# Performance work log

Hardware: AMD Instinct MI355X
Metric: run time of the kernel (lower is better)

Reference implementation:

```python
import jax, jax.numpy as jnp
import numpy as np

N_U = 8192
N_C = 8192
D_IN = 32
D_HID = 32  # hidden_dim == output_dim (required by the concat->Linear shape)


def _glorot(key, fan_in, fan_out):
    r = np.sqrt(6.0 / (fan_in + fan_out)).astype(np.float32)
    return jax.random.uniform(key, (fan_in, fan_out), jnp.float32, -r, r)


def setup_inputs() -> dict:
    key = jax.random.key(0)
    ks = jax.random.split(key, 12)
    X_U = jax.random.normal(ks[0], (N_U, D_IN), jnp.float32)
    X_C = jax.random.normal(ks[1], (N_C, D_IN), jnp.float32)
    adj_uu = jax.random.uniform(ks[2], (N_U, N_U), jnp.float32)
    adj_uc = jax.random.uniform(ks[3], (N_U, N_C), jnp.float32)
    adj_cc = jax.random.uniform(ks[4], (N_C, N_C), jnp.float32)
    weight_s = _glorot(ks[5], D_IN, D_HID)          # GCN_S.weight (shared for uu and cc)
    proj_u = _glorot(ks[6], D_IN, D_HID)            # GCN_C.projection_u
    proj_c = _glorot(ks[7], D_IN, D_HID)            # GCN_C.projection_c (unused in fwd math)
    weight_c = _glorot(ks[8], D_HID, D_HID)         # GCN_C.weight
    W_lin = jax.random.normal(ks[9], (D_IN + D_HID, D_HID), jnp.float32) * 0.05  # Linear, no bias
    a_vec = jax.random.normal(ks[10], (D_HID, 1), jnp.float32) * 0.05            # attention vector
    return {"X_U": X_U, "X_C": X_C, "adj_uu": adj_uu, "adj_uc": adj_uc, "adj_cc": adj_cc,
            "weight_s": weight_s, "proj_u": proj_u, "proj_c": proj_c,
            "weight_c": weight_c, "W_lin": W_lin, "a_vec": a_vec}


def gcn_s(adj, x, w):
    # D^-1/2 A D^-1/2 (X W), with D = 1 + rowsum(A); expressed as broadcast scaling
    dinv = jax.lax.rsqrt(1.0 + jnp.sum(adj, axis=1))  # [N]
    support = x @ w                                    # [N, d]
    return dinv[:, None] * (adj @ (dinv[:, None] * support))


def gcn_c(adj, x_u, p_u, w):
    # Du^-1/2 A Dc^-1/2 ((X_U P_u) W); projected_c is computed but unused upstream
    du = jax.lax.rsqrt(jnp.sum(adj, axis=1))  # [N_u]
    dc = jax.lax.rsqrt(jnp.sum(adj, axis=0))  # [N_c]
    support = (x_u @ p_u) @ w                  # [N_u, d]
    return du[:, None] * (adj @ (dc[:, None] * support))  # wait: see note below


def gcn_c_correct(adj, x_u, p_u, w):
    # norm_adj = diag(du) @ adj @ diag(dc)  -> [N_u, N_c]; output = norm_adj @ support ([N_u,d])
    # Actually original multiplies [N_u,N_c] norm_adj by support built from X_U [N_u,d]:
    # this only typechecks when N_u == N_c (as in the repo's usage). We keep that math.
    du = jax.lax.rsqrt(jnp.sum(adj, axis=1))
    dc = jax.lax.rsqrt(jnp.sum(adj, axis=0))
    support = (x_u @ p_u) @ w
    return du[:, None] * (adj @ (dc[:, None] * support))


def reference(X_U, X_C, adj_uu, adj_uc, adj_cc, weight_s, proj_u, proj_c, weight_c, W_lin, a_vec):
    node_embed_u = gcn_s(adj_uu, X_U, weight_s)            # [N_u, d]
    node_embed_c1 = gcn_s(adj_cc, X_C, weight_s)           # [N_c, d]
    node_embed_c2 = gcn_c_correct(adj_uc, X_U, proj_u, weight_c)  # [N_c, d]

    a_tau_1 = jax.nn.relu(jnp.concatenate([node_embed_c1, X_C], axis=-1) @ W_lin) @ a_vec  # [N_c,1]
    a_tau_2 = jax.nn.relu(jnp.concatenate([node_embed_c2, X_C], axis=-1) @ W_lin) @ a_vec  # [N_c,1]
    e_tau = jax.nn.softmax(jnp.concatenate([a_tau_1, a_tau_2], axis=1), axis=1)            # [N_c,2]

    Y_c = e_tau[:, 0:1] * node_embed_c1
    Y_u = e_tau[:, 1:2] * node_embed_c2
    node_embed_c = Y_c + Y_u
    return (node_embed_u, node_embed_c, Y_c, Y_u)
```

## Files before the change

### kernel.cpp

```cpp
#include <hip/hip_runtime.h>
#include <hip/hip_bf16.h>

#define N_NODES 8192

typedef __attribute__((ext_vector_type(8))) short short8;
typedef __attribute__((ext_vector_type(4))) float floatx4;

__device__ inline unsigned short f2bf(float f) {
  unsigned int u = __float_as_uint(f);
  u = (u + 0x7FFFu + ((u >> 16) & 1u)) >> 16;
  return (unsigned short)u;
}

__device__ inline short8 cvt8(const float4 lo, const float4 hi) {
  short8 r;
  r[0] = (short)f2bf(lo.x); r[1] = (short)f2bf(lo.y);
  r[2] = (short)f2bf(lo.z); r[3] = (short)f2bf(lo.w);
  r[4] = (short)f2bf(hi.x); r[5] = (short)f2bf(hi.y);
  r[6] = (short)f2bf(hi.z); r[7] = (short)f2bf(hi.w);
  return r;
}

__device__ inline float waveSum(float s) {
#pragma unroll
  for (int off = 32; off >= 1; off >>= 1) s += __shfl_xor(s, off, 64);
  return s;
}

__device__ inline void acc4(float4& a, const float4 b) {
  a.x += b.x; a.y += b.y; a.z += b.z; a.w += b.w;
}
__device__ inline float hsum4(const float4 v) { return v.x + v.y + v.z + v.w; }

__global__ __launch_bounds__(256) void k_rowsum(const float* __restrict__ A,
                                                float* __restrict__ dv) {
  int w = threadIdx.x >> 6, l = threadIdx.x & 63;
  long row = (long)blockIdx.x * 4 + w;
  const float* rp = A + row * N_NODES + 4 * l;
  float s = 0.f;
#pragma unroll 2
  for (int i = 0; i < 32; i += 4) {
    float4 v0 = *(const float4*)(rp + 256 * (i + 0));
    float4 v1 = *(const float4*)(rp + 256 * (i + 1));
    float4 v2 = *(const float4*)(rp + 256 * (i + 2));
    float4 v3 = *(const float4*)(rp + 256 * (i + 3));
    s += hsum4(v0) + hsum4(v1) + hsum4(v2) + hsum4(v3);
  }
  s = waveSum(s);
  if (l == 0) dv[row] = rsqrtf(1.0f + s);
}

__global__ __launch_bounds__(256) void k_uc_partials(const float* __restrict__ adj,
                                                     float* __restrict__ rs_part,
                                                     float* __restrict__ cs_part) {
  __shared__ float cacc[4][1024];
  int t = threadIdx.x, w = t >> 6, l = t & 63;
  int rc = blockIdx.x, cc = blockIdx.y;
  int c0 = cc * 1024;
  int rbase = rc * 128 + w * 32;
  float4 ca0 = {0, 0, 0, 0}, ca1 = {0, 0, 0, 0}, ca2 = {0, 0, 0, 0}, ca3 = {0, 0, 0, 0};
  for (int kr = 0; kr < 32; kr += 2) {
    const float* p0 = adj + (long)(rbase + kr) * N_NODES + c0 + 4 * l;
    const float* p1 = p0 + N_NODES;
    float4 u0 = *(const float4*)(p0 + 0);
    float4 u1 = *(const float4*)(p0 + 256);
    float4 u2 = *(const float4*)(p0 + 512);
    float4 u3 = *(const float4*)(p0 + 768);
    float4 v0 = *(const float4*)(p1 + 0);
    float4 v1 = *(const float4*)(p1 + 256);
    float4 v2 = *(const float4*)(p1 + 512);
    float4 v3 = *(const float4*)(p1 + 768);
    acc4(ca0, u0); acc4(ca1, u1); acc4(ca2, u2); acc4(ca3, u3);
    acc4(ca0, v0); acc4(ca1, v1); acc4(ca2, v2); acc4(ca3, v3);
    float s0 = hsum4(u0) + hsum4(u1) + hsum4(u2) + hsum4(u3);
    float s1 = hsum4(v0) + hsum4(v1) + hsum4(v2) + hsum4(v3);
    s0 = waveSum(s0);
    s1 = waveSum(s1);
    if (l == 0) {
      rs_part[(long)cc * N_NODES + rbase + kr] = s0;
      rs_part[(long)cc * N_NODES + rbase + kr + 1] = s1;
    }
  }
  *(float4*)&cacc[w][0 + 4 * l] = ca0;
  *(float4*)&cacc[w][256 + 4 * l] = ca1;
  *(float4*)&cacc[w][512 + 4 * l] = ca2;
  *(float4*)&cacc[w][768 + 4 * l] = ca3;
  __syncthreads();
#pragma unroll
  for (int i = 0; i < 4; ++i) {
    int c = t + 256 * i;
    cs_part[(long)rc * N_NODES + c0 + c] = cacc[0][c] + cacc[1][c] + cacc[2][c] + cacc[3][c];
  }
}

__global__ __launch_bounds__(256) void k_finalize(const float* __restrict__ rs_part,
                                                  const float* __restrict__ cs_part,
                                                  float* __restrict__ du,
                                                  float* __restrict__ dc) {
  int i = blockIdx.x * 256 + threadIdx.x;
  float s = 0.f;
#pragma unroll
  for (int cc = 0; cc < 8; ++cc) s += rs_part[(long)cc * N_NODES + i];
  du[i] = rsqrtf(s);
  float c = 0.f;
#pragma unroll
  for (int rc = 0; rc < 64; ++rc) c += cs_part[(long)rc * N_NODES + i];
  dc[i] = rsqrtf(c);
}

__global__ void k_projw(const float* __restrict__ proj_u,
                        const float* __restrict__ weight_c, float* __restrict__ P) {
  int t = threadIdx.x;
  int i = t >> 5, j = t & 31;
  float s = 0.f;
#pragma unroll
  for (int k = 0; k < 32; ++k) s += proj_u[i * 32 + k] * weight_c[k * 32 + j];
  P[t] = s;
}

__global__ __launch_bounds__(256) void k_support(const float* __restrict__ X,
                                                 const float* __restrict__ W,
                                                 const float* __restrict__ dv,
                                                 short* __restrict__ bt) {
  __shared__ float Wl[32][32];
  __shared__ float Xl[8][32];
  int t = threadIdx.x;
#pragma unroll
  for (int i = 0; i < 4; ++i) {
    int idx = t + 256 * i;
    Wl[idx >> 5][idx & 31] = W[idx];
  }
  int r = t >> 5, n = t & 31;
  int j0 = blockIdx.x * 8;
  Xl[r][n] = X[(long)(j0 + r) * 32 + n];
  __syncthreads();
  float s = 0.f;
#pragma unroll
  for (int k = 0; k < 32; ++k) s += Xl[r][k] * Wl[k][n];
  s *= dv[j0 + r];
  bt[(long)n * N_NODES + j0 + r] = (short)f2bf(s);
}

__global__ __launch_bounds__(64) void k_gemm_wave(const float* __restrict__ adj,
                                                  const short* __restrict__ bt,
                                                  float* __restrict__ part) {
  int l = threadIdx.x;
  int bx = blockIdx.x;
  int kh = bx & 1;
  long r0 = (long)(bx >> 1) * 16;
  int m = l & 15, q = l >> 4;

  const float* ap = adj + (r0 + m) * N_NODES + kh * 4096 + q * 8;
  const short* b0p = bt + (long)m * N_NODES + kh * 4096 + q * 8;
  const short* b1p = b0p + 16L * N_NODES;

  floatx4 acc0 = {0.f, 0.f, 0.f, 0.f}, acc1 = {0.f, 0.f, 0.f, 0.f};

  float4 c0lo = *(const float4*)(ap + 0);
  float4 c0hi = *(const float4*)(ap + 4);
  short8 d00 = *(const short8*)(b0p + 0);
  short8 d10 = *(const short8*)(b1p + 0);
  float4 c1lo = *(const float4*)(ap + 32);
  float4 c1hi = *(const float4*)(ap + 36);
  short8 d01 = *(const short8*)(b0p + 32);
  short8 d11 = *(const short8*)(b1p + 32);

  for (int it = 0; it < 63; ++it) {
    ap += 64; b0p += 64; b1p += 64;
    short8 af0 = cvt8(c0lo, c0hi);
    acc0 = __builtin_amdgcn_mfma_f32_16x16x32_bf16(af0, d00, acc0, 0, 0, 0);
    acc1 = __builtin_amdgcn_mfma_f32_16x16x32_bf16(af0, d10, acc1, 0, 0, 0);
    c0lo = *(const float4*)(ap + 0);
    c0hi = *(const float4*)(ap + 4);
    d00 = *(const short8*)(b0p + 0);
    d10 = *(const short8*)(b1p + 0);
    short8 af1 = cvt8(c1lo, c1hi);
    acc0 = __builtin_amdgcn_mfma_f32_16x16x32_bf16(af1, d01, acc0, 0, 0, 0);
    acc1 = __builtin_amdgcn_mfma_f32_16x16x32_bf16(af1, d11, acc1, 0, 0, 0);
    c1lo = *(const float4*)(ap + 32);
    c1hi = *(const float4*)(ap + 36);
    d01 = *(const short8*)(b0p + 32);
    d11 = *(const short8*)(b1p + 32);
  }
  {
    short8 af0 = cvt8(c0lo, c0hi);
    acc0 = __builtin_amdgcn_mfma_f32_16x16x32_bf16(af0, d00, acc0, 0, 0, 0);
    acc1 = __builtin_amdgcn_mfma_f32_16x16x32_bf16(af0, d10, acc1, 0, 0, 0);
    short8 af1 = cvt8(c1lo, c1hi);
    acc0 = __builtin_amdgcn_mfma_f32_16x16x32_bf16(af1, d01, acc0, 0, 0, 0);
    acc1 = __builtin_amdgcn_mfma_f32_16x16x32_bf16(af1, d11, acc1, 0, 0, 0);
  }

  float* pp = part + (long)kh * 262144 + (r0 + q * 4) * 32;
#pragma unroll
  for (int r = 0; r < 4; ++r) {
    pp[r * 32 + m] = acc0[r];
    pp[r * 32 + 16 + m] = acc1[r];
  }
}

__global__ __launch_bounds__(256) void k_epilogue(
    const float* __restrict__ pu, const float* __restrict__ pc,
    const float* __restrict__ pq, const float* __restrict__ dinv_uu,
    const float* __restrict__ dinv_cc, const float* __restrict__ du,
    const float* __restrict__ X_C, const float* __restrict__ W_lin,
    const float* __restrict__ a_vec, float* __restrict__ out) {
  __shared__ float Wl[64][32];
  __shared__ float al[32];
  int t = threadIdx.x;
#pragma unroll
  for (int i = 0; i < 8; ++i) {
    int idx = t + 256 * i;
    Wl[idx >> 5][idx & 31] = W_lin[idx];
  }
  if (t < 32) al[t] = a_vec[t];
  int g = t >> 5, n = t & 31;
  long row = (long)blockIdx.x * 8 + g;
  long o = row * 32 + n;
  __syncthreads();

  out[o] = dinv_uu[row] * (pu[o] + pu[262144 + o]);

  float h1 = dinv_cc[row] * (pc[o] + pc[262144 + o]);
  float h2 = du[row] * (pq[o] + pq[262144 + o]);
  float xv = X_C[o];
  float s1 = 0.f, s2 = 0.f, sx = 0.f;
#pragma unroll
  for (int k = 0; k < 32; ++k) {
    float h1k = __shfl(h1, k, 32);
    float h2k = __shfl(h2, k, 32);
    float xk = __shfl(xv, k, 32);
    float w0 = Wl[k][n], w1 = Wl[32 + k][n];
    s1 += h1k * w0;
    s2 += h2k * w0;
    sx += xk * w1;
  }
  float t1 = fmaxf(s1 + sx, 0.f) * al[n];
  float t2 = fmaxf(s2 + sx, 0.f) * al[n];
#pragma unroll
  for (int off = 16; off >= 1; off >>= 1) {
    t1 += __shfl_xor(t1, off, 32);
    t2 += __shfl_xor(t2, off, 32);
  }
  float mx = fmaxf(t1, t2);
  float e1 = expf(t1 - mx), e2 = expf(t2 - mx);
  float inv = 1.0f / (e1 + e2);
  float yc = e1 * inv * h1, yu = e2 * inv * h2;
  out[262144 + o] = yc + yu;
  out[524288 + o] = yc;
  out[786432 + o] = yu;
}

extern "C" void kernel_launch(void* const* d_in, const int* in_sizes, int n_in,
                              void* d_out, int out_size, void* d_ws, size_t ws_size,
                              hipStream_t stream) {
  (void)in_sizes; (void)n_in; (void)out_size; (void)ws_size;
  const float* X_U = (const float*)d_in[0];
  const float* X_C = (const float*)d_in[1];
  const float* adj_uu = (const float*)d_in[2];
  const float* adj_uc = (const float*)d_in[3];
  const float* adj_cc = (const float*)d_in[4];
  const float* weight_s = (const float*)d_in[5];
  const float* proj_u = (const float*)d_in[6];
  const float* weight_c = (const float*)d_in[8];
  const float* W_lin = (const float*)d_in[9];
  const float* a_vec = (const float*)d_in[10];
  float* out = (float*)d_out;

  char* ws = (char*)d_ws;
  auto alloc = [&](size_t bytes) {
    char* p = ws;
    ws += (bytes + 255) & ~(size_t)255;
    return p;
  };
  float* dinv_uu = (float*)alloc(8192 * 4);
  float* dinv_cc = (float*)alloc(8192 * 4);
  float* du = (float*)alloc(8192 * 4);
  float* dc = (float*)alloc(8192 * 4);
  float* rs_part = (float*)alloc((size_t)8 * 8192 * 4);
  float* cs_part = (float*)alloc((size_t)64 * 8192 * 4);
  float* P = (float*)alloc(1024 * 4);
  float* pu = (float*)alloc((size_t)2 * 262144 * 4);
  float* pc = (float*)alloc((size_t)2 * 262144 * 4);
  float* pq = (float*)alloc((size_t)2 * 262144 * 4);
  short* bt_uu = (short*)alloc((size_t)262144 * 2);
  short* bt_cc = (short*)alloc((size_t)262144 * 2);
  short* bt_uc = (short*)alloc((size_t)262144 * 2);

  hipLaunchKernelGGL(k_projw, dim3(1), dim3(1024), 0, stream, proj_u, weight_c, P);

  hipLaunchKernelGGL(k_rowsum, dim3(2048), dim3(256), 0, stream, adj_uu, dinv_uu);
  hipLaunchKernelGGL(k_support, dim3(1024), dim3(256), 0, stream,
                     X_U, weight_s, dinv_uu, bt_uu);
  hipLaunchKernelGGL(k_gemm_wave, dim3(1024), dim3(64), 0, stream, adj_uu, bt_uu, pu);

  hipLaunchKernelGGL(k_rowsum, dim3(2048), dim3(256), 0, stream, adj_cc, dinv_cc);
  hipLaunchKernelGGL(k_support, dim3(1024), dim3(256), 0, stream,
                     X_C, weight_s, dinv_cc, bt_cc);
  hipLaunchKernelGGL(k_gemm_wave, dim3(1024), dim3(64), 0, stream, adj_cc, bt_cc, pc);

  hipLaunchKernelGGL(k_uc_partials, dim3(64, 8), dim3(256), 0, stream,
                     adj_uc, rs_part, cs_part);
  hipLaunchKernelGGL(k_finalize, dim3(32), dim3(256), 0, stream,
                     rs_part, cs_part, du, dc);
  hipLaunchKernelGGL(k_support, dim3(1024), dim3(256), 0, stream, X_U, P, dc, bt_uc);
  hipLaunchKernelGGL(k_gemm_wave, dim3(1024), dim3(64), 0, stream, adj_uc, bt_uc, pq);

  hipLaunchKernelGGL(k_epilogue, dim3(1024), dim3(256), 0, stream,
                     pu, pc, pq, dinv_uu, dinv_cc, du, X_C, W_lin, a_vec, out);
}
```

Measured before the change: 877.8 us.

## Batch the three graph branches into single fused degree, support and GEMM launches

Merges the per-adjacency kernels into one launch per stage. The row-sum and uc row/col partial passes run in one grid, the three support builds (including the proj_u·weight_c product and dc finalization) run in one 2D grid, and the three MFMA GEMMs run in one 768-block grid with four waves per block. The du finalize moves into the epilogue. This cuts the launch count from 12 to 4 and fills the GPU with concurrent work across branches. In exchange it adds branch divergence per block and some redundant recomputation, such as the 32x32 projection in every uc support block and the column-sum reduction per row.

```diff
diff --git a/kernel.cpp b/kernel.cpp
--- a/kernel.cpp
+++ b/kernel.cpp
@@ -32,35 +32,39 @@
 }
 __device__ inline float hsum4(const float4 v) { return v.x + v.y + v.z + v.w; }
 
-__global__ __launch_bounds__(256) void k_rowsum(const float* __restrict__ A,
-                                                float* __restrict__ dv) {
-  int w = threadIdx.x >> 6, l = threadIdx.x & 63;
-  long row = (long)blockIdx.x * 4 + w;
-  const float* rp = A + row * N_NODES + 4 * l;
-  float s = 0.f;
+__global__ __launch_bounds__(256) void k_degrees(
+    const float* __restrict__ adj_uu, const float* __restrict__ adj_cc,
+    const float* __restrict__ adj_uc, float* __restrict__ dinv_uu,
+    float* __restrict__ dinv_cc, float* __restrict__ rs_part,
+    float* __restrict__ cs_part) {
+  __shared__ float cacc[4][1024];
+  int b = blockIdx.x;
+  int t = threadIdx.x, w = t >> 6, l = t & 63;
+  if (b < 4096) {
+    const float* A = (b < 2048) ? adj_uu : adj_cc;
+    float* dv = (b < 2048) ? dinv_uu : dinv_cc;
+    long row = (long)(b & 2047) * 4 + w;
+    const float* rp = A + row * N_NODES + 4 * l;
+    float s = 0.f;
 #pragma unroll 2
-  for (int i = 0; i < 32; i += 4) {
-    float4 v0 = *(const float4*)(rp + 256 * (i + 0));
-    float4 v1 = *(const float4*)(rp + 256 * (i + 1));
-    float4 v2 = *(const float4*)(rp + 256 * (i + 2));
-    float4 v3 = *(const float4*)(rp + 256 * (i + 3));
-    s += hsum4(v0) + hsum4(v1) + hsum4(v2) + hsum4(v3);
-  }
-  s = waveSum(s);
-  if (l == 0) dv[row] = rsqrtf(1.0f + s);
-}
-
-__global__ __launch_bounds__(256) void k_uc_partials(const float* __restrict__ adj,
-                                                     float* __restrict__ rs_part,
-                                                     float* __restrict__ cs_part) {
-  __shared__ float cacc[4][1024];
-  int t = threadIdx.x, w = t >> 6, l = t & 63;
-  int rc = blockIdx.x, cc = blockIdx.y;
+    for (int i = 0; i < 32; i += 4) {
+      float4 v0 = *(const float4*)(rp + 256 * (i + 0));
+      float4 v1 = *(const float4*)(rp + 256 * (i + 1));
+      float4 v2 = *(const float4*)(rp + 256 * (i + 2));
+      float4 v3 = *(const float4*)(rp + 256 * (i + 3));
+      s += hsum4(v0) + hsum4(v1) + hsum4(v2) + hsum4(v3);
+    }
+    s = waveSum(s);
+    if (l == 0) dv[row] = rsqrtf(1.0f + s);
+    return;
+  }
+  int idx = b - 4096;
+  int rc = idx & 63, cc = idx >> 6;
   int c0 = cc * 1024;
   int rbase = rc * 128 + w * 32;
   float4 ca0 = {0, 0, 0, 0}, ca1 = {0, 0, 0, 0}, ca2 = {0, 0, 0, 0}, ca3 = {0, 0, 0, 0};
   for (int kr = 0; kr < 32; kr += 2) {
-    const float* p0 = adj + (long)(rbase + kr) * N_NODES + c0 + 4 * l;
+    const float* p0 = adj_uc + (long)(rbase + kr) * N_NODES + c0 + 4 * l;
     const float* p1 = p0 + N_NODES;
     float4 u0 = *(const float4*)(p0 + 0);
     float4 u1 = *(const float4*)(p0 + 256);
@@ -93,61 +97,76 @@
   }
 }
 
-__global__ __launch_bounds__(256) void k_finalize(const float* __restrict__ rs_part,
-                                                  const float* __restrict__ cs_part,
-                                                  float* __restrict__ du,
-                                                  float* __restrict__ dc) {
-  int i = blockIdx.x * 256 + threadIdx.x;
-  float s = 0.f;
-#pragma unroll
-  for (int cc = 0; cc < 8; ++cc) s += rs_part[(long)cc * N_NODES + i];
-  du[i] = rsqrtf(s);
-  float c = 0.f;
-#pragma unroll
-  for (int rc = 0; rc < 64; ++rc) c += cs_part[(long)rc * N_NODES + i];
-  dc[i] = rsqrtf(c);
-}
-
-__global__ void k_projw(const float* __restrict__ proj_u,
-                        const float* __restrict__ weight_c, float* __restrict__ P) {
+__global__ __launch_bounds__(256) void k_support(
+    const float* __restrict__ X_U, const float* __restrict__ X_C,
+    const float* __restrict__ weight_s, const float* __restrict__ proj_u,
+    const float* __restrict__ weight_c, const float* __restrict__ dinv_uu,
+    const float* __restrict__ dinv_cc, const float* __restrict__ cs_part,
+    short* __restrict__ bt_uu, short* __restrict__ bt_cc,
+    short* __restrict__ bt_uc) {
+  int m = blockIdx.y;
+  __shared__ float W1[32][32];
+  __shared__ float W2[32][32];
+  __shared__ float Xl[8][32];
+  __shared__ float Tl[8][32];
   int t = threadIdx.x;
-  int i = t >> 5, j = t & 31;
-  float s = 0.f;
-#pragma unroll
-  for (int k = 0; k < 32; ++k) s += proj_u[i * 32 + k] * weight_c[k * 32 + j];
-  P[t] = s;
-}
-
-__global__ __launch_bounds__(256) void k_support(const float* __restrict__ X,
-                                                 const float* __restrict__ W,
-                                                 const float* __restrict__ dv,
-                                                 short* __restrict__ bt) {
-  __shared__ float Wl[32][32];
-  __shared__ float Xl[8][32];
-  int t = threadIdx.x;
+  const float* X = (m == 1) ? X_C : X_U;
+  const float* Wa = (m == 2) ? proj_u : weight_s;
 #pragma unroll
   for (int i = 0; i < 4; ++i) {
     int idx = t + 256 * i;
-    Wl[idx >> 5][idx & 31] = W[idx];
+    W1[idx >> 5][idx & 31] = Wa[idx];
+  }
+  if (m == 2) {
+#pragma unroll
+    for (int i = 0; i < 4; ++i) {
+      int idx = t + 256 * i;
+      W2[idx >> 5][idx & 31] = weight_c[idx];
+    }
   }
   int r = t >> 5, n = t & 31;
   int j0 = blockIdx.x * 8;
-  Xl[r][n] = X[(long)(j0 + r) * 32 + n];
+  int j = j0 + r;
+  Xl[r][n] = X[(long)j * 32 + n];
   __syncthreads();
   float s = 0.f;
 #pragma unroll
-  for (int k = 0; k < 32; ++k) s += Xl[r][k] * Wl[k][n];
-  s *= dv[j0 + r];
-  bt[(long)n * N_NODES + j0 + r] = (short)f2bf(s);
-}
-
-__global__ __launch_bounds__(64) void k_gemm_wave(const float* __restrict__ adj,
-                                                  const short* __restrict__ bt,
-                                                  float* __restrict__ part) {
-  int l = threadIdx.x;
-  int bx = blockIdx.x;
-  int kh = bx & 1;
-  long r0 = (long)(bx >> 1) * 16;
+  for (int k = 0; k < 32; ++k) s += Xl[r][k] * W1[k][n];
+  float dv;
+  if (m == 0) {
+    dv = dinv_uu[j];
+  } else if (m == 1) {
+    dv = dinv_cc[j];
+  } else {
+    Tl[r][n] = s;
+    __syncthreads();
+    s = 0.f;
+#pragma unroll
+    for (int k = 0; k < 32; ++k) s += Tl[r][k] * W2[k][n];
+    float p = cs_part[(long)n * N_NODES + j] + cs_part[(long)(n + 32) * N_NODES + j];
+#pragma unroll
+    for (int off = 16; off >= 1; off >>= 1) p += __shfl_xor(p, off, 32);
+    dv = rsqrtf(p);
+  }
+  short* bt = (m == 0) ? bt_uu : (m == 1) ? bt_cc : bt_uc;
+  bt[(long)n * N_NODES + j] = (short)f2bf(s * dv);
+}
+
+__global__ __launch_bounds__(256) void k_gemm(
+    const float* __restrict__ adj_uu, const float* __restrict__ adj_cc,
+    const float* __restrict__ adj_uc, const short* __restrict__ bt_uu,
+    const short* __restrict__ bt_cc, const short* __restrict__ bt_uc,
+    float* __restrict__ pu, float* __restrict__ pc, float* __restrict__ pq) {
+  int b = blockIdx.x;
+  int mm = b >> 8;
+  const float* adj = (mm == 0) ? adj_uu : (mm == 1) ? adj_cc : adj_uc;
+  const short* bt = (mm == 0) ? bt_uu : (mm == 1) ? bt_cc : bt_uc;
+  float* part = (mm == 0) ? pu : (mm == 1) ? pc : pq;
+
+  int w = threadIdx.x >> 6, l = threadIdx.x & 63;
+  int g = (b & 255) * 4 + w;
+  int kh = g & 1;
+  long r0 = (long)(g >> 1) * 16;
   int m = l & 15, q = l >> 4;
 
   const float* ap = adj + (r0 + m) * N_NODES + kh * 4096 + q * 8;
@@ -202,7 +221,7 @@
 __global__ __launch_bounds__(256) void k_epilogue(
     const float* __restrict__ pu, const float* __restrict__ pc,
     const float* __restrict__ pq, const float* __restrict__ dinv_uu,
-    const float* __restrict__ dinv_cc, const float* __restrict__ du,
+    const float* __restrict__ dinv_cc, const float* __restrict__ rs_part,
     const float* __restrict__ X_C, const float* __restrict__ W_lin,
     const float* __restrict__ a_vec, float* __restrict__ out) {
   __shared__ float Wl[64][32];
@@ -221,8 +240,13 @@
 
   out[o] = dinv_uu[row] * (pu[o] + pu[262144 + o]);
 
+  float sdu = 0.f;
+#pragma unroll
+  for (int cc = 0; cc < 8; ++cc) sdu += rs_part[(long)cc * N_NODES + row];
+  float du = rsqrtf(sdu);
+
   float h1 = dinv_cc[row] * (pc[o] + pc[262144 + o]);
-  float h2 = du[row] * (pq[o] + pq[262144 + o]);
+  float h2 = du * (pq[o] + pq[262144 + o]);
   float xv = X_C[o];
   float s1 = 0.f, s2 = 0.f, sx = 0.f;
 #pragma unroll
@@ -275,11 +299,8 @@
   };
   float* dinv_uu = (float*)alloc(8192 * 4);
   float* dinv_cc = (float*)alloc(8192 * 4);
-  float* du = (float*)alloc(8192 * 4);
-  float* dc = (float*)alloc(8192 * 4);
   float* rs_part = (float*)alloc((size_t)8 * 8192 * 4);
   float* cs_part = (float*)alloc((size_t)64 * 8192 * 4);
-  float* P = (float*)alloc(1024 * 4);
   float* pu = (float*)alloc((size_t)2 * 262144 * 4);
   float* pc = (float*)alloc((size_t)2 * 262144 * 4);
   float* pq = (float*)alloc((size_t)2 * 262144 * 4);
@@ -287,25 +308,13 @@
   short* bt_cc = (short*)alloc((size_t)262144 * 2);
   short* bt_uc = (short*)alloc((size_t)262144 * 2);
 
-  hipLaunchKernelGGL(k_projw, dim3(1), dim3(1024), 0, stream, proj_u, weight_c, P);
-
-  hipLaunchKernelGGL(k_rowsum, dim3(2048), dim3(256), 0, stream, adj_uu, dinv_uu);
-  hipLaunchKernelGGL(k_support, dim3(1024), dim3(256), 0, stream,
-                     X_U, weight_s, dinv_uu, bt_uu);
-  hipLaunchKernelGGL(k_gemm_wave, dim3(1024), dim3(64), 0, stream, adj_uu, bt_uu, pu);
-
-  hipLaunchKernelGGL(k_rowsum, dim3(2048), dim3(256), 0, stream, adj_cc, dinv_cc);
-  hipLaunchKernelGGL(k_support, dim3(1024), dim3(256), 0, stream,
-                     X_C, weight_s, dinv_cc, bt_cc);
-  hipLaunchKernelGGL(k_gemm_wave, dim3(1024), dim3(64), 0, stream, adj_cc, bt_cc, pc);
-
-  hipLaunchKernelGGL(k_uc_partials, dim3(64, 8), dim3(256), 0, stream,
-                     adj_uc, rs_part, cs_part);
-  hipLaunchKernelGGL(k_finalize, dim3(32), dim3(256), 0, stream,
-                     rs_part, cs_part, du, dc);
-  hipLaunchKernelGGL(k_support, dim3(1024), dim3(256), 0, stream, X_U, P, dc, bt_uc);
-  hipLaunchKernelGGL(k_gemm_wave, dim3(1024), dim3(64), 0, stream, adj_uc, bt_uc, pq);
-
+  hipLaunchKernelGGL(k_degrees, dim3(4608), dim3(256), 0, stream,
+                     adj_uu, adj_cc, adj_uc, dinv_uu, dinv_cc, rs_part, cs_part);
+  hipLaunchKernelGGL(k_support, dim3(1024, 3), dim3(256), 0, stream,
+                     X_U, X_C, weight_s, proj_u, weight_c, dinv_uu, dinv_cc,
+                     cs_part, bt_uu, bt_cc, bt_uc);
+  hipLaunchKernelGGL(k_gemm, dim3(768), dim3(256), 0, stream,
+                     adj_uu, adj_cc, adj_uc, bt_uu, bt_cc, bt_uc, pu, pc, pq);
   hipLaunchKernelGGL(k_epilogue, dim3(1024), dim3(256), 0, stream,
-                     pu, pc, pq, dinv_uu, dinv_cc, du, X_C, W_lin, a_vec, out);
-}
+                     pu, pc, pq, dinv_uu, dinv_cc, rs_part, X_C, W_lin, a_vec, out);
+}
```

Result: no change. 877.3 us (-0.1%).
